# Performance work log

Hardware: AMD Instinct MI355X
Metric: run time of the kernel (lower is better)

The kernel has to match this reference:

```python
import math
import jax, jax.numpy as jnp
import numpy as np

D_MODEL = 1024
N_HEADS = 16
D_HEAD = D_MODEL // N_HEADS
B, T = 2, 2048


def setup_inputs() -> dict:
    key = jax.random.key(0)
    k1, k2, k3, k4, k5 = jax.random.split(key, 5)
    s = 1.0 / math.sqrt(D_MODEL)
    x = jax.random.normal(k1, (B, T, D_MODEL), dtype=jnp.float32)
    w_qkv = jax.random.normal(k2, (D_MODEL, 3 * D_MODEL), dtype=jnp.float32) * s
    b_qkv = jnp.zeros((3 * D_MODEL,), dtype=jnp.float32)
    w_out = jax.random.normal(k3, (D_MODEL, D_MODEL), dtype=jnp.float32) * s
    b_out = jnp.zeros((D_MODEL,), dtype=jnp.float32)
    # causal mask, broadcastable to [B, H, T, T]; 0 -> masked
    attn_mask = jnp.tril(jnp.ones((T, T), dtype=jnp.int32))[None, None]
    return {"x": x, "w_qkv": w_qkv, "b_qkv": b_qkv, "w_out": w_out,
            "b_out": b_out, "attn_mask": attn_mask}


def reference(x, w_qkv, b_qkv, w_out, b_out, attn_mask):
    Bsz, Tlen, C = x.shape
    qkv = x @ w_qkv + b_qkv                       # [B, T, 3C]
    q, k, v = jnp.split(qkv, 3, axis=-1)

    def reshape(t):
        return t.reshape(Bsz, Tlen, N_HEADS, D_HEAD).transpose(0, 2, 1, 3)

    q, k, v = reshape(q), reshape(k), reshape(v)  # [B, H, T, d]
    scores = jnp.einsum("bhqd,bhkd->bhqk", q, k) / math.sqrt(D_HEAD)
    scores = jnp.where(attn_mask == 0, -jnp.inf, scores)
    w = jax.nn.softmax(scores, axis=-1)
    y = jnp.einsum("bhqk,bhkd->bhqd", w, v)       # [B, H, T, d]
    y = y.transpose(0, 2, 1, 3).reshape(Bsz, Tlen, C)
    return y @ w_out + b_out
```

## Files before the change

kernel.cpp:

```cpp
#include <hip/hip_runtime.h>
#include <hip/hip_bf16.h>
#include <stdint.h>


typedef __bf16 bf16_t;
typedef __bf16 bf16x8 __attribute__((ext_vector_type(8)));
typedef __bf16 bf16x4 __attribute__((ext_vector_type(4)));
typedef short  s16x4  __attribute__((ext_vector_type(4)));
typedef float  f32x4  __attribute__((ext_vector_type(4)));

#define SEQ   2048
#define DM    1024
#define NH    16
#define DH    64
#define BATCH 2

__device__ __forceinline__ bf16x8 load8(const bf16_t* p) {
    return *reinterpret_cast<const bf16x8*>(p);
}
__device__ __forceinline__ f32x4 loadf4(const float* p) {
    return *reinterpret_cast<const f32x4*>(p);
}
__device__ __forceinline__ void async16(const bf16_t* g, bf16_t* lds_base) {
    __builtin_amdgcn_global_load_lds(
        (const __attribute__((address_space(1))) void*)g,
        (__attribute__((address_space(3))) void*)lds_base, 16, 0, 0);
}
__device__ __forceinline__ float fast_exp2(float x) {
#if __has_builtin(__builtin_amdgcn_exp2f)
    return __builtin_amdgcn_exp2f(x);
#else
    return __expf(x * 0.69314718056f);
#endif
}
__device__ __forceinline__ int swz(int row, int chunk) {
    return row * 64 + ((chunk ^ (row & 7)) * 8);
}

__device__ __forceinline__ void tcvt_tile(
    const float* __restrict__ w, bf16_t* __restrict__ wT, int N,
    int n0, int k0, bf16_t (*tile)[65])
{
    const int tid = threadIdx.x;
#pragma unroll
    for (int i = 0; i < 4; ++i) {
        const int r = i * 16 + (tid >> 4);
        const int c = (tid & 15) * 4;
        f32x4 v = loadf4(w + (size_t)(k0 + r) * N + n0 + c);
#pragma unroll
        for (int j = 0; j < 4; ++j) tile[c + j][r] = (bf16_t)v[j];
    }
    __syncthreads();
#pragma unroll
    for (int i = 0; i < 4; ++i) {
        const int r = i * 16 + (tid >> 4);
        const int c = (tid & 15) * 4;
        ushort4 v;
        v.x = *(const uint16_t*)&tile[r][c];
        v.y = *(const uint16_t*)&tile[r][c + 1];
        v.z = *(const uint16_t*)&tile[r][c + 2];
        v.w = *(const uint16_t*)&tile[r][c + 3];
        *reinterpret_cast<ushort4*>(wT + (size_t)(n0 + r) * DM + k0 + c) = v;
    }
}

__global__ __launch_bounds__(256) void pre_kernel(
    const float* __restrict__ x, bf16_t* __restrict__ xb,
    const float* __restrict__ w_qkv, bf16_t* __restrict__ wqkvT)
{
    __shared__ bf16_t tile[64][65];
    const int bid = blockIdx.x;
    if (bid < 2048) {
        const int i = (bid * 256 + threadIdx.x) * 8;
        f32x4 a = loadf4(x + i);
        f32x4 b = loadf4(x + i + 4);
        bf16x8 v;
#pragma unroll
        for (int j = 0; j < 4; ++j) { v[j] = (bf16_t)a[j]; v[4 + j] = (bf16_t)b[j]; }
        *reinterpret_cast<bf16x8*>(xb + i) = v;
    } else {
        const int t = bid - 2048;
        tcvt_tile(w_qkv, wqkvT, 3072, (t % 48) * 64, (t / 48) * 64, tile);
    }
}

__global__ __launch_bounds__(256) void tcvt_kernel(
    const float* __restrict__ w, bf16_t* __restrict__ wT, int N)
{
    __shared__ bf16_t tile[64][65];
    tcvt_tile(w, wT, N, blockIdx.x * 64, blockIdx.y * 64, tile);
}

template <typename TA, int MODE, int NT>
__global__ __launch_bounds__(256) void gemm_bt_kernel(
    const TA* __restrict__ A, const bf16_t* __restrict__ BT,
    const float* __restrict__ bias,
    float* __restrict__ outF,
    bf16_t* __restrict__ oq, bf16_t* __restrict__ ok, bf16_t* __restrict__ ov)
{
    constexpr int SAS = (sizeof(TA) == 4) ? 72 : 64;
    constexpr int NB  = NT / 32;
    __shared__ bf16_t sA[128 * SAS];
    __shared__ bf16_t sB[NT * 64];

    const int tid  = threadIdx.x;
    const int lane = tid & 63;
    const int wv   = tid >> 6;
    const int lq   = lane >> 4;
    const int lm   = lane & 15;
    const int wm   = (wv >> 1) * 64;
    const int wn   = (wv & 1) * (NT / 2);

    const int flat = blockIdx.y * gridDim.x + blockIdx.x;
    const int cls  = flat & 7;
    const int q8   = flat >> 3;
    const int mb   = (cls + 8 * (q8 & 3)) * 128;
    const int nb   = (q8 >> 2) * NT;

    const int srow = lane >> 3;
    const int scol = (lane & 7) * 8;
    const int scs  = ((lane & 7) ^ srow) * 8;

    f32x4 acc[4][NB];
#pragma unroll
    for (int a = 0; a < 4; ++a)
#pragma unroll
        for (int b = 0; b < NB; ++b) acc[a][b] = f32x4{0.f, 0.f, 0.f, 0.f};

    for (int it = 0; it < 16; ++it) {
        const int k0 = it * 64;
        if constexpr (sizeof(TA) == 4) {
            const int arow = tid >> 1;
            const int akc  = (tid & 1) * 32;
            const float* g = (const float*)A + (size_t)(mb + arow) * DM + k0 + akc;
            bf16_t* dst = &sA[arow * SAS + akc];
#pragma unroll
            for (int j = 0; j < 4; ++j) {
                f32x4 u0 = loadf4(g + j * 8);
                f32x4 u1 = loadf4(g + j * 8 + 4);
                bf16x8 w;
#pragma unroll
                for (int e = 0; e < 4; ++e) { w[e] = (bf16_t)u0[e]; w[4 + e] = (bf16_t)u1[e]; }
                *reinterpret_cast<bf16x8*>(dst + j * 8) = w;
            }
        } else {
#pragma unroll
            for (int r = 0; r < 4; ++r) {
                const int row = wv * 32 + r * 8 + srow;
                async16((const bf16_t*)A + (size_t)(mb + row) * DM + k0 + scs,
                        &sA[wv * 2048 + r * 512]);
            }
        }
#pragma unroll
        for (int r = 0; r < NT / 32; ++r) {
            const int row = wv * (NT / 4) + r * 8 + srow;
            async16(BT + (size_t)(nb + row) * DM + k0 + scs,
                    &sB[wv * (NT / 4) * 64 + r * 512]);
        }
        __syncthreads();
#pragma unroll
        for (int kh = 0; kh < 2; ++kh) {
            bf16x8 af[4], bfr[NB];
#pragma unroll
            for (int a = 0; a < 4; ++a) {
                if constexpr (sizeof(TA) == 4)
                    af[a] = load8(&sA[(wm + a * 16 + lm) * SAS + kh * 32 + lq * 8]);
                else
                    af[a] = load8(&sA[swz(wm + a * 16 + lm, kh * 4 + lq)]);
            }
#pragma unroll
            for (int b = 0; b < NB; ++b)
                bfr[b] = load8(&sB[swz(wn + b * 16 + lm, kh * 4 + lq)]);
#pragma unroll
            for (int a = 0; a < 4; ++a)
#pragma unroll
                for (int b = 0; b < NB; ++b)
                    acc[a][b] = __builtin_amdgcn_mfma_f32_16x16x32_bf16(
                        af[a], bfr[b], acc[a][b], 0, 0, 0);
        }
        __syncthreads();
    }

#pragma unroll
    for (int b = 0; b < NB; ++b) {
        const int n = nb + wn + b * 16 + lm;
        const float bv = bias[n];
        if (MODE == 0) {
            const int which = n >> 10;
            const int cc = n & 1023;
            const int h  = cc >> 6;
            const int d  = cc & 63;
            if (which == 2) {
#pragma unroll
                for (int a = 0; a < 4; ++a) {
                    const int m0 = mb + wm + a * 16 + lq * 4;
                    const int bb = m0 >> 11;
                    const int t0 = m0 & 2047;
                    bf16x4 w;
#pragma unroll
                    for (int r = 0; r < 4; ++r) w[r] = (bf16_t)(acc[a][b][r] + bv);
                    *reinterpret_cast<bf16x4*>(
                        ov + ((size_t)(bb * NH + h) * DH + d) * SEQ + t0) = w;
                }
            } else {
                bf16_t* dst = (which == 0) ? oq : ok;
#pragma unroll
                for (int a = 0; a < 4; ++a)
#pragma unroll
                    for (int r = 0; r < 4; ++r) {
                        const int m = mb + wm + a * 16 + lq * 4 + r;
                        const int bb = m >> 11;
                        const int t  = m & 2047;
                        dst[((size_t)(bb * NH + h) * SEQ + t) * DH + d] =
                            (bf16_t)(acc[a][b][r] + bv);
                    }
            }
        } else {
#pragma unroll
            for (int a = 0; a < 4; ++a)
#pragma unroll
                for (int r = 0; r < 4; ++r) {
                    const int m = mb + wm + a * 16 + lq * 4 + r;
                    outF[(size_t)m * DM + n] = acc[a][b][r] + bv;
                }
        }
    }
}

__global__ __launch_bounds__(256) void attn_kernel(
    const bf16_t* __restrict__ qbuf, const bf16_t* __restrict__ kbuf,
    const bf16_t* __restrict__ vtbuf, bf16_t* __restrict__ ybuf,
    bf16_t* __restrict__ p1, float* __restrict__ l0buf,
    float* __restrict__ l1buf, int split)
{
    __shared__ bf16_t sK[2][2 * 64 * 64];
    __shared__ bf16_t sVt[2][2 * 64 * 64];

    const int tid  = threadIdx.x;
    const int lane = tid & 63;
    const int wv   = tid >> 6;
    const int lq   = lane >> 4;
    const int lm   = lane & 15;

    const int p    = blockIdx.y * gridDim.x + blockIdx.x;
    const int slot = p >> 3;
    const int bh   = (p & 7) + ((slot & 3) << 3);
    const int uid  = slot >> 2;

    int qi, kt0, ktn, chunk1;
    if (!split)        { qi = 15 - uid;        kt0 = 0;  ktn = 2 * qi + 2;      chunk1 = 0; }
    else if (uid < 9)  { qi = 15 - uid;        kt0 = 0;  ktn = 16;              chunk1 = 0; }
    else if (uid < 17) { qi = 15 - (uid - 9);  kt0 = 16; ktn = 2 * qi + 2 - 16; chunk1 = 1; }
    else               { qi = 6 - (uid - 17);  kt0 = 0;  ktn = 2 * qi + 2;      chunk1 = 0; }
    const bool fin = !split || (!chunk1 && qi < 8);
    const int q_base = qi * 128;
    const int nps = ktn >> 1;

    const size_t hb = (size_t)bh * SEQ * DH;
    const bf16_t* Q  = qbuf + hb;
    const bf16_t* K  = kbuf + hb;
    const bf16_t* VT = vtbuf + hb;

    bf16x8 qf0[2], qf1[2];
#pragma unroll
    for (int ms = 0; ms < 2; ++ms) {
        const bf16_t* p_ = Q + (size_t)(q_base + wv * 32 + ms * 16 + lm) * DH + lq * 8;
        qf0[ms] = load8(p_);
        qf1[ms] = load8(p_ + 32);
    }

    f32x4 o[2][4];
    float ls[2];
#pragma unroll
    for (int ms = 0; ms < 2; ++ms) {
        ls[ms] = 0.f;
#pragma unroll
        for (int dc = 0; dc < 4; ++dc) o[ms][dc] = f32x4{0.f, 0.f, 0.f, 0.f};
    }

    const int srow = lane >> 3;
    const int scs  = ((lane & 7) ^ srow) * 8;

    {
        const int kb0 = kt0 * 64;
#pragma unroll
        for (int hf = 0; hf < 2; ++hf)
#pragma unroll
            for (int r = 0; r < 2; ++r) {
                async16(K + (size_t)(kb0 + hf * 64 + wv * 16 + r * 8 + srow) * DH + scs,
                        &sK[0][hf * 4096 + wv * 1024 + r * 512]);
                async16(VT + (size_t)(wv * 16 + r * 8 + srow) * SEQ + kb0 + hf * 64 + scs,
                        &sVt[0][hf * 4096 + wv * 1024 + r * 512]);
            }
    }
    __syncthreads();

    const float c1 = 0.125f * 1.44269504f;
    const float c2 = 10.0f  * 1.44269504f;

    for (int sp = 0; sp < nps; ++sp) {
        const int cb = sp & 1, nbuf = cb ^ 1;
        if (sp + 1 < nps) {
            const int kb2 = (kt0 + (sp + 1) * 2) * 64;
#pragma unroll
            for (int hf = 0; hf < 2; ++hf)
#pragma unroll
                for (int r = 0; r < 2; ++r) {
                    async16(K + (size_t)(kb2 + hf * 64 + wv * 16 + r * 8 + srow) * DH + scs,
                            &sK[nbuf][hf * 4096 + wv * 1024 + r * 512]);
                    async16(VT + (size_t)(wv * 16 + r * 8 + srow) * SEQ + kb2 + hf * 64 + scs,
                            &sVt[nbuf][hf * 4096 + wv * 1024 + r * 512]);
                }
        }

#pragma unroll
        for (int hf = 0; hf < 2; ++hf) {
            const int kb = (kt0 + sp * 2 + hf) * 64;
            const bf16_t* sKc = &sK[cb][hf * 4096];
            const bf16_t* sVc = &sVt[cb][hf * 4096];

            bf16x8 kf0[4], kf1[4];
#pragma unroll
            for (int c = 0; c < 4; ++c) {
                kf0[c] = load8(&sKc[swz(c * 16 + lm, lq)]);
                kf1[c] = load8(&sKc[swz(c * 16 + lm, lq + 4)]);
            }
            s16x4 vf[4][4];
#pragma unroll
            for (int dc = 0; dc < 4; ++dc)
#pragma unroll
                for (int c = 0; c < 4; ++c)
                    vf[dc][c] = *reinterpret_cast<const s16x4*>(
                        &sVc[swz(dc * 16 + lm, c * 2 + (lq >> 1)) + (lq & 1) * 4]);

#pragma unroll
            for (int ms = 0; ms < 2; ++ms) {
                const int rowlo = wv * 32 + ms * 16;
                if (q_base + rowlo + 15 < kb) continue;

                f32x4 s[4];
#pragma unroll
                for (int c = 0; c < 4; ++c) {
                    f32x4 z = f32x4{0.f, 0.f, 0.f, 0.f};
                    f32x4 t0 = __builtin_amdgcn_mfma_f32_16x16x32_bf16(kf0[c], qf0[ms], z, 0, 0, 0);
                    s[c] = __builtin_amdgcn_mfma_f32_16x16x32_bf16(kf1[c], qf1[ms], t0, 0, 0, 0);
                }

                const int q = q_base + rowlo + lm;
                float p4[4][4];
                if (kb + 63 > q_base + rowlo) {
#pragma unroll
                    for (int c = 0; c < 4; ++c)
#pragma unroll
                        for (int r = 0; r < 4; ++r) {
                            const int key = kb + c * 16 + lq * 4 + r;
                            float t = (key <= q) ? fmaf(s[c][r], c1, -c2) : -1e30f;
                            p4[c][r] = fast_exp2(t);
                        }
                } else {
#pragma unroll
                    for (int c = 0; c < 4; ++c)
#pragma unroll
                        for (int r = 0; r < 4; ++r)
                            p4[c][r] = fast_exp2(fmaf(s[c][r], c1, -c2));
                }
                float lsum = 0.f;
#pragma unroll
                for (int c = 0; c < 4; ++c)
                    lsum += (p4[c][0] + p4[c][1]) + (p4[c][2] + p4[c][3]);
                ls[ms] += lsum;

                s16x4 pf[4];
#pragma unroll
                for (int c = 0; c < 4; ++c) {
                    bf16x4 v;
#pragma unroll
                    for (int r = 0; r < 4; ++r) v[r] = (bf16_t)p4[c][r];
                    pf[c] = __builtin_bit_cast(s16x4, v);
                }

#pragma unroll
                for (int dc = 0; dc < 4; ++dc)
#pragma unroll
                    for (int c = 0; c < 4; ++c)
                        o[ms][dc] = __builtin_amdgcn_mfma_f32_16x16x16bf16_1k(
                            vf[dc][c], pf[c], o[ms][dc], 0, 0, 0);
            }
        }

        __syncthreads();
    }

    __syncthreads();
    bf16_t* sT = &sK[0][0];
    const int b = bh >> 4;
    const int h = bh & 15;
#pragma unroll
    for (int ms = 0; ms < 2; ++ms) {
        float l = ls[ms];
        l += __shfl_xor(l, 16);
        l += __shfl_xor(l, 32);
        const float inv = fin ? (1.0f / l) : 1.0f;
        if (!fin && lq == 0) {
            const int q = q_base + wv * 32 + ms * 16 + lm;
            float* lb = chunk1 ? l1buf : l0buf;
            lb[bh * 1024 + (q - 1024)] = l;
        }
#pragma unroll
        for (int dc = 0; dc < 4; ++dc)
#pragma unroll
            for (int r = 0; r < 4; ++r)
                sT[wv * 1152 + lm * 72 + dc * 16 + lq * 4 + r] =
                    (bf16_t)(o[ms][dc][r] * inv);
        const int t = q_base + wv * 32 + ms * 16 + (lane & 15);
        const bf16_t* src = &sT[wv * 1152 + (lane & 15) * 72 + (lane >> 4) * 16];
        bf16x8 y0 = load8(src);
        bf16x8 y1 = load8(src + 8);
        bf16_t* dst;
        if (chunk1)
            dst = p1 + ((size_t)(bh * 1024 + (t - 1024))) * 64 + (lane >> 4) * 16;
        else
            dst = ybuf + ((size_t)(b * SEQ + t)) * DM + h * DH + (lane >> 4) * 16;
        *reinterpret_cast<bf16x8*>(dst)     = y0;
        *reinterpret_cast<bf16x8*>(dst + 8) = y1;
    }
}

__global__ __launch_bounds__(256) void post_kernel(
    bf16_t* __restrict__ yb, const bf16_t* __restrict__ p1,
    const float* __restrict__ l0, const float* __restrict__ l1,
    const float* __restrict__ w_out, bf16_t* __restrict__ woutT)
{
    __shared__ bf16_t tile[64][65];
    const int bid = blockIdx.x;
    if (bid < 1024) {
        const int idx = bid * 256 + threadIdx.x;
        const int d8  = (idx & 7) * 8;
        const int row = idx >> 3;
        const int ql  = row & 1023;
        const int bh  = row >> 10;
        const int q   = 1024 + ql;
        const int b   = bh >> 4, h = bh & 15;
        const float inv = 1.0f / (l0[row] + l1[row]);
        bf16_t* yp = yb + ((size_t)(b * SEQ + q)) * DM + h * DH + d8;
        const bf16_t* pp = p1 + (size_t)row * 64 + d8;
        bf16x8 a = load8(yp), c = load8(pp);
        bf16x8 oo;
#pragma unroll
        for (int j = 0; j < 8; ++j)
            oo[j] = (bf16_t)(((float)a[j] + (float)c[j]) * inv);
        *reinterpret_cast<bf16x8*>(yp) = oo;
    } else {
        const int t = bid - 1024;
        tcvt_tile(w_out, woutT, 1024, (t % 16) * 64, (t / 16) * 64, tile);
    }
}

extern "C" void kernel_launch(void* const* d_in, const int* in_sizes, int n_in,
                              void* d_out, int out_size, void* d_ws, size_t ws_size,
                              hipStream_t stream)
{
    const float* x     = (const float*)d_in[0];
    const float* w_qkv = (const float*)d_in[1];
    const float* b_qkv = (const float*)d_in[2];
    const float* w_out = (const float*)d_in[3];
    const float* b_out = (const float*)d_in[4];
    float* out = (float*)d_out;

    char* ws = (char*)d_ws;
    bf16_t* qb = (bf16_t*)(ws);
    bf16_t* kb = (bf16_t*)(ws + (8u << 20));
    bf16_t* vb = (bf16_t*)(ws + (16u << 20));
    bf16_t* yb = (bf16_t*)(ws + (24u << 20));
    bf16_t* woutT = qb;

    const bool bigws = (ws_size >= ((size_t)38 << 20));

    if (bigws) {
        bf16_t* xb    = yb;
        bf16_t* wqkvT = (bf16_t*)(ws + (32u << 20));
        pre_kernel<<<dim3(2048 + 768), dim3(256), 0, stream>>>(x, xb, w_qkv, wqkvT);
        gemm_bt_kernel<bf16_t, 0, 128><<<dim3(3072 / 128, 4096 / 128), dim3(256), 0, stream>>>(
            xb, wqkvT, b_qkv, nullptr, qb, kb, vb);

        bf16_t* p1 = (bf16_t*)(ws + (32u << 20));
        float*  l0 = (float*)(ws + (36u << 20));
        float*  l1 = (float*)(ws + (36u << 20) + (128u << 10));
        attn_kernel<<<dim3(24, BATCH * NH), dim3(256), 0, stream>>>(
            qb, kb, vb, yb, p1, l0, l1, 1);
        post_kernel<<<dim3(1024 + 256), dim3(256), 0, stream>>>(
            yb, p1, l0, l1, w_out, woutT);
    } else {
        bf16_t* wqkvT = yb;
        tcvt_kernel<<<dim3(3072 / 64, 1024 / 64), dim3(256), 0, stream>>>(w_qkv, wqkvT, 3072);
        gemm_bt_kernel<float, 0, 128><<<dim3(3072 / 128, 4096 / 128), dim3(256), 0, stream>>>(
            x, wqkvT, b_qkv, nullptr, qb, kb, vb);
        attn_kernel<<<dim3(16, BATCH * NH), dim3(256), 0, stream>>>(
            qb, kb, vb, yb, yb, nullptr, nullptr, 0);
        tcvt_kernel<<<dim3(1024 / 64, 1024 / 64), dim3(256), 0, stream>>>(w_out, woutT, 1024);
    }

    gemm_bt_kernel<bf16_t, 1, 64><<<dim3(1024 / 64, 4096 / 128), dim3(256), 0, stream>>>(
        yb, woutT, b_out, out, nullptr, nullptr, nullptr);
}
```

Measured before the change: 185.3 us.

## Double attention query tile to 256 rows with 512-thread blocks and MFMA priority

The attention kernel now gives each block 256 query rows across 8 waves instead of 128 rows across 4. Each K/V LDS tile is therefore reused by twice as many waves, cutting global-to-LDS traffic per query, and the causal split schedule and grid sizes are reworked to match. It also raises wave priority around the MFMA sections so matrix work issues ahead of the exp/softmax work of other waves. The cost is half as many blocks, which may leave compute units underused and worsen load imbalance across the causal triangle.

```diff
diff --git a/kernel.cpp b/kernel.cpp
--- a/kernel.cpp
+++ b/kernel.cpp
@@ -227,7 +227,7 @@
     }
 }
 
-__global__ __launch_bounds__(256) void attn_kernel(
+__global__ __launch_bounds__(512) void attn_kernel(
     const bf16_t* __restrict__ qbuf, const bf16_t* __restrict__ kbuf,
     const bf16_t* __restrict__ vtbuf, bf16_t* __restrict__ ybuf,
     bf16_t* __restrict__ p1, float* __restrict__ l0buf,
@@ -248,12 +248,12 @@
     const int uid  = slot >> 2;
 
     int qi, kt0, ktn, chunk1;
-    if (!split)        { qi = 15 - uid;        kt0 = 0;  ktn = 2 * qi + 2;      chunk1 = 0; }
-    else if (uid < 9)  { qi = 15 - uid;        kt0 = 0;  ktn = 16;              chunk1 = 0; }
-    else if (uid < 17) { qi = 15 - (uid - 9);  kt0 = 16; ktn = 2 * qi + 2 - 16; chunk1 = 1; }
-    else               { qi = 6 - (uid - 17);  kt0 = 0;  ktn = 2 * qi + 2;      chunk1 = 0; }
-    const bool fin = !split || (!chunk1 && qi < 8);
-    const int q_base = qi * 128;
+    if (!split)        { qi = 7 - uid;   kt0 = 0;  ktn = 4 * qi + 4;  chunk1 = 0; }
+    else if (uid < 4)  { qi = 7 - uid;   kt0 = 0;  ktn = 16;          chunk1 = 0; }
+    else if (uid < 8)  { qi = 11 - uid;  kt0 = 16; ktn = 4 * qi - 12; chunk1 = 1; }
+    else               { qi = 11 - uid;  kt0 = 0;  ktn = 4 * qi + 4;  chunk1 = 0; }
+    const bool fin = !split || (!chunk1 && qi < 4);
+    const int q_base = qi * 256;
     const int nps = ktn >> 1;
 
     const size_t hb = (size_t)bh * SEQ * DH;
@@ -284,14 +284,12 @@
     {
         const int kb0 = kt0 * 64;
 #pragma unroll
-        for (int hf = 0; hf < 2; ++hf)
-#pragma unroll
-            for (int r = 0; r < 2; ++r) {
-                async16(K + (size_t)(kb0 + hf * 64 + wv * 16 + r * 8 + srow) * DH + scs,
-                        &sK[0][hf * 4096 + wv * 1024 + r * 512]);
-                async16(VT + (size_t)(wv * 16 + r * 8 + srow) * SEQ + kb0 + hf * 64 + scs,
-                        &sVt[0][hf * 4096 + wv * 1024 + r * 512]);
-            }
+        for (int hf = 0; hf < 2; ++hf) {
+            async16(K + (size_t)(kb0 + hf * 64 + wv * 8 + srow) * DH + scs,
+                    &sK[0][hf * 4096 + wv * 512]);
+            async16(VT + (size_t)(wv * 8 + srow) * SEQ + kb0 + hf * 64 + scs,
+                    &sVt[0][hf * 4096 + wv * 512]);
+        }
     }
     __syncthreads();
 
@@ -303,14 +301,12 @@
         if (sp + 1 < nps) {
             const int kb2 = (kt0 + (sp + 1) * 2) * 64;
 #pragma unroll
-            for (int hf = 0; hf < 2; ++hf)
-#pragma unroll
-                for (int r = 0; r < 2; ++r) {
-                    async16(K + (size_t)(kb2 + hf * 64 + wv * 16 + r * 8 + srow) * DH + scs,
-                            &sK[nbuf][hf * 4096 + wv * 1024 + r * 512]);
-                    async16(VT + (size_t)(wv * 16 + r * 8 + srow) * SEQ + kb2 + hf * 64 + scs,
-                            &sVt[nbuf][hf * 4096 + wv * 1024 + r * 512]);
-                }
+            for (int hf = 0; hf < 2; ++hf) {
+                async16(K + (size_t)(kb2 + hf * 64 + wv * 8 + srow) * DH + scs,
+                        &sK[nbuf][hf * 4096 + wv * 512]);
+                async16(VT + (size_t)(wv * 8 + srow) * SEQ + kb2 + hf * 64 + scs,
+                        &sVt[nbuf][hf * 4096 + wv * 512]);
+            }
         }
 
 #pragma unroll
@@ -339,12 +335,14 @@
                 if (q_base + rowlo + 15 < kb) continue;
 
                 f32x4 s[4];
+                __builtin_amdgcn_s_setprio(1);
 #pragma unroll
                 for (int c = 0; c < 4; ++c) {
                     f32x4 z = f32x4{0.f, 0.f, 0.f, 0.f};
                     f32x4 t0 = __builtin_amdgcn_mfma_f32_16x16x32_bf16(kf0[c], qf0[ms], z, 0, 0, 0);
                     s[c] = __builtin_amdgcn_mfma_f32_16x16x32_bf16(kf1[c], qf1[ms], t0, 0, 0, 0);
                 }
+                __builtin_amdgcn_s_setprio(0);
 
                 const int q = q_base + rowlo + lm;
                 float p4[4][4];
@@ -354,8 +352,8 @@
 #pragma unroll
                         for (int r = 0; r < 4; ++r) {
                             const int key = kb + c * 16 + lq * 4 + r;
-                            float t = (key <= q) ? fmaf(s[c][r], c1, -c2) : -1e30f;
-                            p4[c][r] = fast_exp2(t);
+                            float tt = (key <= q) ? fmaf(s[c][r], c1, -c2) : -1e30f;
+                            p4[c][r] = fast_exp2(tt);
                         }
                 } else {
 #pragma unroll
@@ -379,12 +377,14 @@
                     pf[c] = __builtin_bit_cast(s16x4, v);
                 }
 
+                __builtin_amdgcn_s_setprio(1);
 #pragma unroll
                 for (int dc = 0; dc < 4; ++dc)
 #pragma unroll
                     for (int c = 0; c < 4; ++c)
                         o[ms][dc] = __builtin_amdgcn_mfma_f32_16x16x16bf16_1k(
                             vf[dc][c], pf[c], o[ms][dc], 0, 0, 0);
+                __builtin_amdgcn_s_setprio(0);
             }
         }
 
@@ -486,7 +486,7 @@
         bf16_t* p1 = (bf16_t*)(ws + (32u << 20));
         float*  l0 = (float*)(ws + (36u << 20));
         float*  l1 = (float*)(ws + (36u << 20) + (128u << 10));
-        attn_kernel<<<dim3(24, BATCH * NH), dim3(256), 0, stream>>>(
+        attn_kernel<<<dim3(12, BATCH * NH), dim3(512), 0, stream>>>(
             qb, kb, vb, yb, p1, l0, l1, 1);
         post_kernel<<<dim3(1024 + 256), dim3(256), 0, stream>>>(
             yb, p1, l0, l1, w_out, woutT);
@@ -495,7 +495,7 @@
         tcvt_kernel<<<dim3(3072 / 64, 1024 / 64), dim3(256), 0, stream>>>(w_qkv, wqkvT, 3072);
         gemm_bt_kernel<float, 0, 128><<<dim3(3072 / 128, 4096 / 128), dim3(256), 0, stream>>>(
             x, wqkvT, b_qkv, nullptr, qb, kb, vb);
-        attn_kernel<<<dim3(16, BATCH * NH), dim3(256), 0, stream>>>(
+        attn_kernel<<<dim3(8, 32), dim3(512), 0, stream>>>(
             qb, kb, vb, yb, yb, nullptr, nullptr, 0);
         tcvt_kernel<<<dim3(1024 / 64, 1024 / 64), dim3(256), 0, stream>>>(w_out, woutT, 1024);
     }
```

Result: slower. 189.2 us (+2.1%).
